# Kernel tuning notes

Measured on AMD Instinct MI355X. Metric: run time of the kernel, lower is better.

Reference implementation:

```python
import jax, jax.numpy as jnp
import numpy as np

QLEN, KLEN, BSZ, NHEAD, DHEAD = 1024, 1024, 2, 16, 64
RLEN = QLEN + KLEN
SCALE = 1.0 / np.sqrt(DHEAD).astype(np.float32)  # 1/sqrt(d_head)


def setup_inputs() -> dict:
    key = jax.random.key(0)
    ks = jax.random.split(key, 10)
    return {
        "q_head": jax.random.normal(ks[0], (QLEN, BSZ, NHEAD, DHEAD), jnp.float32),
        "k_head_h": jax.random.normal(ks[1], (KLEN, BSZ, NHEAD, DHEAD), jnp.float32),
        "v_head_h": jax.random.normal(ks[2], (KLEN, BSZ, NHEAD, DHEAD), jnp.float32),
        "k_head_r": jax.random.normal(ks[3], (RLEN, BSZ, NHEAD, DHEAD), jnp.float32),
        "seg_embed": jax.random.normal(ks[4], (2, NHEAD, DHEAD), jnp.float32),
        "seg_mat": jax.random.uniform(ks[5], (QLEN, KLEN, BSZ, 2), jnp.float32),
        "r_w_bias": jax.random.normal(ks[6], (NHEAD, DHEAD), jnp.float32),
        "r_r_bias": jax.random.normal(ks[7], (NHEAD, DHEAD), jnp.float32),
        "r_s_bias": jax.random.normal(ks[8], (NHEAD, DHEAD), jnp.float32),
        "attn_mask": jnp.zeros((QLEN, KLEN, 1, 1), jnp.float32),
    }


def _rel_shift(x, klen):
    # x: [qlen, rlen, bsz, n_head] -> [qlen, klen, bsz, n_head]
    x = jnp.transpose(x, (1, 0, 2, 3))[1:]          # drop first position row
    x = jnp.transpose(x, (1, 0, 2, 3))[:, :klen]    # keep first klen columns
    return x


def reference(q_head, k_head_h, v_head_h, k_head_r, seg_embed, seg_mat,
              r_w_bias, r_r_bias, r_s_bias, attn_mask):
    # content-based score
    ac = jnp.einsum('ibnd,jbnd->ijbn', q_head + r_w_bias, k_head_h)
    # position-based score with relative shift
    bd = jnp.einsum('ibnd,jbnd->ijbn', q_head + r_r_bias, k_head_r)
    bd = _rel_shift(bd, klen=ac.shape[1])
    # segment-based score
    ef = jnp.einsum('ibnd,snd->ibns', q_head + r_s_bias, seg_embed)
    ef = jnp.einsum('ijbs,ibns->ijbn', seg_mat, ef)
    attn_score = (ac + bd + ef) * SCALE
    attn_score = attn_score - 1e30 * attn_mask
    attn_prob = jax.nn.softmax(attn_score, axis=1)  # over key dim j
    attn_vec = jnp.einsum('ijbn,jbnd->ibnd', attn_prob, v_head_h)
    return attn_vec
```

## Files before the change

kernel.cpp:

```cpp
#include <hip/hip_runtime.h>

#define QLEN 1024
#define KLEN 1024
#define BSZ 2
#define NHEAD 16
#define DHEAD 64
#define RS 2048
#define BLK_I 64
#define BLK_J 32
#define NT32 (KLEN / BLK_J)
#define NBN (BSZ * NHEAD)

#define SC2f  0.18033688011112440f
#define MBIGf 1.4426950408889634e30f
#define THRf  8.0f

#define SEGP_BYTES  16777216u
#define KT_BYTES    ((size_t)NBN * NT32 * 4096)
#define OPART_BYTES 16777216u
#define ML_BYTES    524288u

typedef __attribute__((ext_vector_type(8))) short s16x8;
typedef __attribute__((ext_vector_type(4))) short s16x4;
typedef __attribute__((ext_vector_type(8))) unsigned short u16x8;
typedef __attribute__((ext_vector_type(4))) unsigned short u16x4;
typedef __attribute__((ext_vector_type(4))) float f32x4;
typedef __attribute__((ext_vector_type(2))) float f32x2;

__device__ __forceinline__ unsigned short f2bf(float f) {
    union { float f; unsigned int u; } x; x.f = f;
    unsigned int r = x.u + 0x7fffu + ((x.u >> 16) & 1u);
    return (unsigned short)(r >> 16);
}
__device__ __forceinline__ float bf2f(unsigned short h) {
    union { unsigned int u; float f; } x; x.u = ((unsigned int)h) << 16;
    return x.f;
}

__device__ __forceinline__ f32x4 mfma16x16x16(s16x4 a, s16x4 b, f32x4 c) {
#if __has_builtin(__builtin_amdgcn_mfma_f32_16x16x16bf16_1k)
    return __builtin_amdgcn_mfma_f32_16x16x16bf16_1k(a, b, c, 0, 0, 0);
#else
    f32x4 d;
    asm("v_mfma_f32_16x16x16_bf16 %0, %1, %2, %3"
        : "=v"(d) : "v"(a), "v"(b), "0"(c));
    return d;
#endif
}

typedef const __attribute__((address_space(1))) unsigned int* gas_t;
typedef __attribute__((address_space(3))) unsigned int* las_t;
__device__ __forceinline__ void gl_lds16(const void* g, void* l) {
    __builtin_amdgcn_global_load_lds((gas_t)g, (las_t)l, 16, 0, 0);
}

__global__ __launch_bounds__(256)
void pack_all_kernel(const float* __restrict__ segmat,
                     const float* __restrict__ mask,
                     const float* __restrict__ kh,
                     const float* __restrict__ kr,
                     const float* __restrict__ v,
                     unsigned short* __restrict__ segT,
                     unsigned short* __restrict__ Kp,
                     unsigned short* __restrict__ Krp,
                     unsigned short* __restrict__ Vtp)
{
    __shared__ float smS[16][32][4];
    __shared__ float smM[16][33];
    __shared__ float VT[32][65];
    const int bid = blockIdx.x;
    const int tid = threadIdx.x;

    if (bid < 2048) {
        const int istrip = bid >> 5;
        const int jt     = bid & 31;
        const int ib     = istrip * 16;
        const int jb     = jt * 32;
        {
            const int il = tid >> 4;
            const int j2 = (tid & 15) * 2;
            const float* sp = segmat + ((size_t)(ib + il) * KLEN + jb + j2) * 4;
            *(f32x4*)&smS[il][j2][0]     = *(const f32x4*)sp;
            *(f32x4*)&smS[il][j2 + 1][0] = *(const f32x4*)(sp + 4);
            const float* mp = mask + (size_t)(ib + il) * KLEN + jb + j2;
            smM[il][j2]     = mp[0] * MBIGf;
            smM[il][j2 + 1] = mp[1] * MBIGf;
        }
        __syncthreads();
        const int k  = tid >> 6;
        const int l  = tid & 63;
        const int q4 = l >> 4;
        const int il = l & 15;
        const int jl = (k >> 1) * 16 + q4 * 4 + (k & 1) * 2;
#pragma unroll
        for (int b = 0; b < 2; ++b) {
            u16x8 o;
#pragma unroll
            for (int e = 0; e < 2; ++e) {
                o[e * 4 + 0] = f2bf(smS[il][jl + e][b * 2]);
                o[e * 4 + 1] = f2bf(smS[il][jl + e][b * 2 + 1]);
                o[e * 4 + 2] = f2bf(smM[il][jl + e]);
                o[e * 4 + 3] = 0;
            }
            unsigned short* op = segT + ((size_t)(b * 64 + istrip) << 16)
                                 + (jt << 11) + tid * 8;
            *(u16x8*)op = o;
        }
    } else {
        const int blk = bid - 2048;
        const int bn  = blk >> 5;
        const int jt  = blk & (NT32 - 1);
        const int b   = bn & 1;
        const int n   = bn >> 1;
        const int boff = b * NHEAD * DHEAD + n * DHEAD;
        const int j0  = jt * BLK_J;

        {
            const int j  = tid >> 3;
            const int dq = (tid & 7) * 8;
            const float* vp = v + (size_t)(j0 + j) * RS + boff + dq;
#pragma unroll
            for (int e = 0; e < 8; ++e) VT[j][dq + e] = vp[e];
        }
        __syncthreads();

        const size_t tb = (size_t)blk * 2048;
        {
            const int row = tid >> 3;
            const int ch  = (tid & 7) ^ (row & 7);
            u16x8 ok, orr;
            const float* hp = kh + (size_t)(j0 + row) * RS + boff + ch * 8;
            const float* rp = kr + (size_t)(j0 + row + 1) * RS + boff + ch * 8;
#pragma unroll
            for (int e = 0; e < 8; ++e) { ok[e] = f2bf(hp[e]); orr[e] = f2bf(rp[e]); }
            *(u16x8*)&Kp [tb + (size_t)tid * 8] = ok;
            *(u16x8*)&Krp[tb + (size_t)tid * 8] = orr;
        }
        {
            const int d  = tid >> 2;
            const int g  = tid & 3;
            const int ch = g ^ (d & 3);
            u16x8 ov;
#pragma unroll
            for (int e = 0; e < 8; ++e) ov[e] = f2bf(VT[ch * 8 + e][d]);
            *(u16x8*)&Vtp[tb + (size_t)tid * 8] = ov;
        }
    }
}

__global__ __launch_bounds__(256)
void merge_kernel(const float* __restrict__ opart,
                  const float* __restrict__ ml,
                  float* __restrict__ out)
{
    const int gid = blockIdx.x * 256 + threadIdx.x;
    const int d   = gid & 63;
    const int rr  = gid >> 6;
    const int i   = rr & (QLEN - 1);
    const int n   = (rr >> 10) & (NHEAD - 1);
    const int b   = rr >> 14;
    const int r0  = rr;
    const int r1  = (NBN * QLEN) + rr;
    const float m0 = ml[r0 * 2], l0 = ml[r0 * 2 + 1];
    const float m1 = ml[r1 * 2], l1 = ml[r1 * 2 + 1];
    const float M  = fmaxf(m0, m1);
    const float w0 = __builtin_amdgcn_exp2f(m0 - M);
    const float w1 = __builtin_amdgcn_exp2f(m1 - M);
    const float inv = 1.f / (l0 * w0 + l1 * w1);
    const float o = (opart[(size_t)r0 * 64 + d] * w0 + opart[(size_t)r1 * 64 + d] * w1) * inv;
    out[(size_t)i * RS + b * NHEAD * DHEAD + n * DHEAD + d] = o;
}

__global__ __launch_bounds__(256, 4)
void relattn_kernel(const float* __restrict__ q,
                    const float* __restrict__ segemb,
                    const float* __restrict__ rwb,
                    const float* __restrict__ rrb,
                    const float* __restrict__ rsb,
                    const unsigned short* __restrict__ segT,
                    const unsigned short* __restrict__ Kp,
                    const unsigned short* __restrict__ Krp,
                    const unsigned short* __restrict__ Vtp,
                    float* __restrict__ opart,
                    float* __restrict__ mlpart,
                    float* __restrict__ out,
                    int jsplit, int njt)
{
    __shared__ unsigned short KhL[2][32][64];
    __shared__ unsigned short KrL[2][32][64];
    __shared__ unsigned short VtL[2][64][32];

    const int F = blockIdx.x;
    const int x = F & 7;
    const int k = F >> 3;
    const int g = (k >> 4) * 8 + x;
    const int n = k & 15;
    int i0, b, jsp;
    if (jsplit) { i0 = (g >> 2) * BLK_I; b = (g >> 1) & 1; jsp = g & 1; }
    else        { i0 = (g >> 1) * BLK_I; b = g & 1;        jsp = 0;    }
    const int bn = n * 2 + b;
    const int boff = b * NHEAD * DHEAD + n * DHEAD;

    const int tid  = threadIdx.x;
    const int wave = tid >> 6;
    const int lane = tid & 63;
    const int q4   = lane >> 4;
    const int c    = lane & 15;
    const int iRow = i0 + wave * 16 + c;

    s16x8 qwf[2], qrf[2];
    float e0, e1;
    {
        const float* qp = q + (size_t)iRow * RS + boff;
        float es0 = 0.f, es1 = 0.f;
#pragma unroll
        for (int kk = 0; kk < 2; ++kk) {
            const int off = kk * 32 + q4 * 8;
            const f32x4 q0 = *(const f32x4*)(qp + off);
            const f32x4 q1 = *(const f32x4*)(qp + off + 4);
            const f32x4 w0 = *(const f32x4*)(rwb + n * DHEAD + off);
            const f32x4 w1 = *(const f32x4*)(rwb + n * DHEAD + off + 4);
            const f32x4 r0 = *(const f32x4*)(rrb + n * DHEAD + off);
            const f32x4 r1 = *(const f32x4*)(rrb + n * DHEAD + off + 4);
            const f32x4 sa = *(const f32x4*)(segemb + n * DHEAD + off);
            const f32x4 sb = *(const f32x4*)(segemb + n * DHEAD + off + 4);
            const f32x4 ta = *(const f32x4*)(segemb + (NHEAD + n) * DHEAD + off);
            const f32x4 tb = *(const f32x4*)(segemb + (NHEAD + n) * DHEAD + off + 4);
            const f32x4 ra = *(const f32x4*)(rsb + n * DHEAD + off);
            const f32x4 rb = *(const f32x4*)(rsb + n * DHEAD + off + 4);
            s16x8 tw, tr;
#pragma unroll
            for (int e = 0; e < 4; ++e) {
                tw[e]     = (short)f2bf(q0[e] + w0[e]);
                tw[4 + e] = (short)f2bf(q1[e] + w1[e]);
                tr[e]     = (short)f2bf(q0[e] + r0[e]);
                tr[4 + e] = (short)f2bf(q1[e] + r1[e]);
                es0 += (q0[e] + ra[e]) * sa[e] + (q1[e] + rb[e]) * sb[e];
                es1 += (q0[e] + ra[e]) * ta[e] + (q1[e] + rb[e]) * tb[e];
            }
            qwf[kk] = tw; qrf[kk] = tr;
        }
        es0 += __shfl_xor(es0, 16, 64); es0 += __shfl_xor(es0, 32, 64);
        es1 += __shfl_xor(es1, 16, 64); es1 += __shfl_xor(es1, 32, 64);
        e0 = es0 * SC2f; e1 = es1 * SC2f;
    }

    const int tbase = bn * NT32 + jsp * njt;
    auto stage = [&](int jt, int buf) {
        const size_t toff = ((size_t)(tbase + jt)) << 12;
        const int go = tid * 16;
        const int lo = wave * 1024;
        gl_lds16((const char*)Kp  + toff + go, (char*)&KhL[buf][0][0] + lo);
        gl_lds16((const char*)Krp + toff + go, (char*)&KrL[buf][0][0] + lo);
        gl_lds16((const char*)Vtp + toff + go, (char*)&VtL[buf][0][0] + lo);
    };

    stage(0, 0);
    __syncthreads();

    float m = -INFINITY, lsum = 0.f;
    f32x4 acc[4];
#pragma unroll
    for (int dt = 0; dt < 4; ++dt) acc[dt] = (f32x4)0.f;

    const unsigned short* segW = segT + ((size_t)(b * 64 + (i0 >> 4) + wave) << 16);

    int cur = 0;
    for (int jt = 0; jt < njt; ++jt) {
        if (jt + 1 < njt) stage(jt + 1, cur ^ 1);

        const unsigned short* st = segW + ((jsp * njt + jt) << 11);
        u16x8 pg[2][2];
        pg[0][0] = *(const u16x8*)(st + lane * 8);
        pg[0][1] = *(const u16x8*)(st + 512 + lane * 8);
        pg[1][0] = *(const u16x8*)(st + 1024 + lane * 8);
        pg[1][1] = *(const u16x8*)(st + 1536 + lane * 8);

        f32x4 sjT[2];
        sjT[0] = (f32x4)0.f; sjT[1] = (f32x4)0.f;
        __builtin_amdgcn_s_setprio(1);
#pragma unroll
        for (int kk = 0; kk < 2; ++kk)
#pragma unroll
            for (int js = 0; js < 2; ++js) {
                const int row = js * 16 + c;
                const int pcK = ((kk * 4 + q4) ^ (c & 7)) * 8;
                const s16x8 khf = *(const s16x8*)&KhL[cur][row][pcK];
                const s16x8 krf = *(const s16x8*)&KrL[cur][row][pcK];
                sjT[js] = __builtin_amdgcn_mfma_f32_16x16x32_bf16(khf, qwf[kk], sjT[js], 0, 0, 0);
                sjT[js] = __builtin_amdgcn_mfma_f32_16x16x32_bf16(krf, qrf[kk], sjT[js], 0, 0, 0);
            }
        __builtin_amdgcn_s_setprio(0);

        float sc8[8];
#pragma unroll
        for (int js = 0; js < 2; ++js)
#pragma unroll
            for (int r = 0; r < 4; ++r) {
                const u16x8 g2 = pg[js][r >> 1];
                const int bb = (r & 1) * 4;
                sc8[js * 4 + r] = sjT[js][r] * SC2f
                                  + bf2f(g2[bb]) * e0 + bf2f(g2[bb + 1]) * e1
                                  - bf2f(g2[bb + 2]);
            }
        float pmax = fmaxf(
            fmaxf(fmaxf(sc8[0], sc8[1]), fmaxf(sc8[2], sc8[3])),
            fmaxf(fmaxf(sc8[4], sc8[5]), fmaxf(sc8[6], sc8[7])));

        if (!__all(pmax <= m + THRf)) {
            float mt = pmax;
            mt = fmaxf(mt, __shfl_xor(mt, 16, 64));
            mt = fmaxf(mt, __shfl_xor(mt, 32, 64));
            const float mn  = fmaxf(m, mt);
            const float scl = __builtin_amdgcn_exp2f(m - mn);
            m = mn;
            lsum *= scl;
#pragma unroll
            for (int dt = 0; dt < 4; ++dt) acc[dt] *= scl;
        }

        float p[8], ps = 0.f;
#pragma unroll
        for (int e = 0; e < 8; ++e) {
            p[e] = __builtin_amdgcn_exp2f(sc8[e] - m);
            ps += p[e];
        }
        lsum += ps;

        s16x4 pf4[2];
#pragma unroll
        for (int js = 0; js < 2; ++js) {
            union { unsigned int w[2]; s16x4 v; } pk;
            asm("v_cvt_pk_bf16_f32 %0, %1, %2" : "=v"(pk.w[0]) : "v"(p[js * 4 + 0]), "v"(p[js * 4 + 1]));
            asm("v_cvt_pk_bf16_f32 %0, %1, %2" : "=v"(pk.w[1]) : "v"(p[js * 4 + 2]), "v"(p[js * 4 + 3]));
            pf4[js] = pk.v;
        }
        __builtin_amdgcn_s_setprio(1);
#pragma unroll
        for (int dt = 0; dt < 4; ++dt) {
            const unsigned short* vrow = &VtL[cur][dt * 16 + c][0];
#pragma unroll
            for (int js = 0; js < 2; ++js) {
                const int gg = (js * 2 + (q4 >> 1)) ^ (c & 3);
                const s16x4 vf = *(const s16x4*)(vrow + gg * 8 + (q4 & 1) * 4);
                acc[dt] = mfma16x16x16(vf, pf4[js], acc[dt]);
            }
        }
        __builtin_amdgcn_s_setprio(0);

        __syncthreads();
        cur ^= 1;
    }

    lsum += __shfl_xor(lsum, 16, 64);
    lsum += __shfl_xor(lsum, 32, 64);

    if (jsplit) {
        const int rowG = ((jsp * BSZ + b) * NHEAD + n) * QLEN + iRow;
#pragma unroll
        for (int dt = 0; dt < 4; ++dt)
            *(f32x4*)&opart[(size_t)rowG * 64 + dt * 16 + q4 * 4] = acc[dt];
        if (q4 == 0) {
            mlpart[(size_t)rowG * 2]     = m;
            mlpart[(size_t)rowG * 2 + 1] = lsum;
        }
    } else {
        const float inv = 1.f / lsum;
        float* op = out + (size_t)iRow * RS + boff;
#pragma unroll
        for (int dt = 0; dt < 4; ++dt) {
            const f32x4 o = acc[dt] * inv;
            *(f32x4*)&op[dt * 16 + q4 * 4] = o;
        }
    }
}

extern "C" void kernel_launch(void* const* d_in, const int* in_sizes, int n_in,
                              void* d_out, int out_size, void* d_ws, size_t ws_size,
                              hipStream_t stream) {
    const float* q   = (const float*)d_in[0];
    const float* kh  = (const float*)d_in[1];
    const float* v   = (const float*)d_in[2];
    const float* kr  = (const float*)d_in[3];
    const float* se  = (const float*)d_in[4];
    const float* sm  = (const float*)d_in[5];
    const float* rwb = (const float*)d_in[6];
    const float* rrb = (const float*)d_in[7];
    const float* rsb = (const float*)d_in[8];
    const float* msk = (const float*)d_in[9];
    float* out = (float*)d_out;

    char* wsb = (char*)d_ws;
    unsigned short* segT = (unsigned short*)wsb;
    unsigned short* Kp   = (unsigned short*)(wsb + SEGP_BYTES);
    unsigned short* Krp  = (unsigned short*)(wsb + SEGP_BYTES + KT_BYTES);
    unsigned short* Vtp  = (unsigned short*)(wsb + SEGP_BYTES + 2 * KT_BYTES);
    float* opart  = (float*)(wsb + SEGP_BYTES + 3 * KT_BYTES);
    float* mlpart = (float*)(wsb + SEGP_BYTES + 3 * KT_BYTES + OPART_BYTES);

    const int jsplit = (ws_size >= (size_t)SEGP_BYTES + 3 * KT_BYTES + OPART_BYTES + ML_BYTES) ? 1 : 0;
    const int njt    = jsplit ? NT32 / 2 : NT32;

    pack_all_kernel<<<2048 + NBN * NT32, 256, 0, stream>>>(sm, msk, kh, kr, v,
                                                           segT, Kp, Krp, Vtp);
    relattn_kernel<<<jsplit ? 1024 : 512, 256, 0, stream>>>(q, se, rwb, rrb, rsb,
                                                            segT, Kp, Krp, Vtp,
                                                            opart, mlpart, out,
                                                            jsplit, njt);
    if (jsplit)
        merge_kernel<<<NBN * QLEN * DHEAD / 256, 256, 0, stream>>>(opart, mlpart, out);
}
```

Before: 59.60 us.

## Triple-buffer K/V tiles with prefetched segment data and fine-grained vmcnt waits

Moves the K/Kr/Vt LDS staging from double to triple buffering, issuing loads two tiles ahead. The segment-matrix loads are now prefetched one tile ahead into alternating register sets. The full __syncthreads is replaced by explicit vmcnt waits plus s_barrier, so outstanding global loads can stay in flight across iterations. It also folds the softmax scale into the bf16 Q operands and re-swizzles the Vt layout to 4-element chunks to change LDS bank conflicts. The costs are more LDS and registers per block, which may lower occupancy, and the hand-counted vmcnt values are fragile. The loop now assumes an even tile count.

```diff
diff --git a/kernel.cpp b/kernel.cpp
--- a/kernel.cpp
+++ b/kernel.cpp
@@ -138,12 +138,16 @@
         }
         {
             const int d  = tid >> 2;
-            const int g  = tid & 3;
-            const int ch = g ^ (d & 3);
-            u16x8 ov;
-#pragma unroll
-            for (int e = 0; e < 8; ++e) ov[e] = f2bf(VT[ch * 8 + e][d]);
-            *(u16x8*)&Vtp[tb + (size_t)tid * 8] = ov;
+            const int gl = tid & 3;
+#pragma unroll
+            for (int s = 0; s < 2; ++s) {
+                const int gj8 = gl * 2 + s;
+                const int ph  = gj8 ^ (d & 7);
+                u16x4 ov;
+#pragma unroll
+                for (int e = 0; e < 4; ++e) ov[e] = f2bf(VT[gj8 * 4 + e][d]);
+                *(u16x4*)&Vtp[tb + (size_t)d * 32 + ph * 4] = ov;
+            }
         }
     }
 }
@@ -186,9 +190,9 @@
                     float* __restrict__ out,
                     int jsplit, int njt)
 {
-    __shared__ unsigned short KhL[2][32][64];
-    __shared__ unsigned short KrL[2][32][64];
-    __shared__ unsigned short VtL[2][64][32];
+    __shared__ unsigned short KhL[3][32][64];
+    __shared__ unsigned short KrL[3][32][64];
+    __shared__ unsigned short VtL[3][64][32];
 
     const int F = blockIdx.x;
     const int x = F & 7;
@@ -231,10 +235,10 @@
             s16x8 tw, tr;
 #pragma unroll
             for (int e = 0; e < 4; ++e) {
-                tw[e]     = (short)f2bf(q0[e] + w0[e]);
-                tw[4 + e] = (short)f2bf(q1[e] + w1[e]);
-                tr[e]     = (short)f2bf(q0[e] + r0[e]);
-                tr[4 + e] = (short)f2bf(q1[e] + r1[e]);
+                tw[e]     = (short)f2bf((q0[e] + w0[e]) * SC2f);
+                tw[4 + e] = (short)f2bf((q1[e] + w1[e]) * SC2f);
+                tr[e]     = (short)f2bf((q0[e] + r0[e]) * SC2f);
+                tr[4 + e] = (short)f2bf((q1[e] + r1[e]) * SC2f);
                 es0 += (q0[e] + ra[e]) * sa[e] + (q1[e] + rb[e]) * sb[e];
                 es1 += (q0[e] + ra[e]) * ta[e] + (q1[e] + rb[e]) * tb[e];
             }
@@ -254,27 +258,40 @@
         gl_lds16((const char*)Krp + toff + go, (char*)&KrL[buf][0][0] + lo);
         gl_lds16((const char*)Vtp + toff + go, (char*)&VtL[buf][0][0] + lo);
     };
-
-    stage(0, 0);
-    __syncthreads();
+    const unsigned short* segW = segT + ((size_t)(b * 64 + (i0 >> 4) + wave) << 16);
+    auto segload = [&](int jt, u16x8 (&pg)[4]) {
+        const unsigned short* st = segW + ((jsp * njt + jt) << 11);
+        pg[0] = *(const u16x8*)(st + lane * 8);
+        pg[1] = *(const u16x8*)(st + 512 + lane * 8);
+        pg[2] = *(const u16x8*)(st + 1024 + lane * 8);
+        pg[3] = *(const u16x8*)(st + 1536 + lane * 8);
+    };
 
     float m = -INFINITY, lsum = 0.f;
     f32x4 acc[4];
 #pragma unroll
     for (int dt = 0; dt < 4; ++dt) acc[dt] = (f32x4)0.f;
 
-    const unsigned short* segW = segT + ((size_t)(b * 64 + (i0 >> 4) + wave) << 16);
+    u16x8 pgA[4], pgB[4];
+    stage(0, 0);
+    __builtin_amdgcn_sched_barrier(0);
+    segload(0, pgA);
+    __builtin_amdgcn_sched_barrier(0);
+    stage(1, 1);
+    __builtin_amdgcn_sched_barrier(0);
+    asm volatile("s_waitcnt vmcnt(7)" ::: "memory");
+    __builtin_amdgcn_s_barrier();
+    __builtin_amdgcn_sched_barrier(0);
 
     int cur = 0;
-    for (int jt = 0; jt < njt; ++jt) {
-        if (jt + 1 < njt) stage(jt + 1, cur ^ 1);
-
-        const unsigned short* st = segW + ((jsp * njt + jt) << 11);
-        u16x8 pg[2][2];
-        pg[0][0] = *(const u16x8*)(st + lane * 8);
-        pg[0][1] = *(const u16x8*)(st + 512 + lane * 8);
-        pg[1][0] = *(const u16x8*)(st + 1024 + lane * 8);
-        pg[1][1] = *(const u16x8*)(st + 1536 + lane * 8);
+    auto body = [&](int t, u16x8 (&pgC)[4], u16x8 (&pgN)[4]) {
+        const int tn1 = (t + 1 < njt) ? t + 1 : njt - 1;
+        const int tn2 = (t + 2 < njt) ? t + 2 : njt - 1;
+        int b2 = cur + 2; if (b2 >= 3) b2 -= 3;
+        segload(tn1, pgN);
+        __builtin_amdgcn_sched_barrier(0);
+        stage(tn2, b2);
+        __builtin_amdgcn_sched_barrier(0);
 
         f32x4 sjT[2];
         sjT[0] = (f32x4)0.f; sjT[1] = (f32x4)0.f;
@@ -297,9 +314,9 @@
         for (int js = 0; js < 2; ++js)
 #pragma unroll
             for (int r = 0; r < 4; ++r) {
-                const u16x8 g2 = pg[js][r >> 1];
+                const u16x8 g2 = pgC[js * 2 + (r >> 1)];
                 const int bb = (r & 1) * 4;
-                sc8[js * 4 + r] = sjT[js][r] * SC2f
+                sc8[js * 4 + r] = sjT[js][r]
                                   + bf2f(g2[bb]) * e0 + bf2f(g2[bb + 1]) * e1
                                   - bf2f(g2[bb + 2]);
             }
@@ -330,10 +347,10 @@
         s16x4 pf4[2];
 #pragma unroll
         for (int js = 0; js < 2; ++js) {
-            union { unsigned int w[2]; s16x4 v; } pk;
-            asm("v_cvt_pk_bf16_f32 %0, %1, %2" : "=v"(pk.w[0]) : "v"(p[js * 4 + 0]), "v"(p[js * 4 + 1]));
-            asm("v_cvt_pk_bf16_f32 %0, %1, %2" : "=v"(pk.w[1]) : "v"(p[js * 4 + 2]), "v"(p[js * 4 + 3]));
-            pf4[js] = pk.v;
+            union { unsigned int w[2]; s16x4 v; } pk2;
+            asm("v_cvt_pk_bf16_f32 %0, %1, %2" : "=v"(pk2.w[0]) : "v"(p[js*4+0]), "v"(p[js*4+1]));
+            asm("v_cvt_pk_bf16_f32 %0, %1, %2" : "=v"(pk2.w[1]) : "v"(p[js*4+2]), "v"(p[js*4+3]));
+            pf4[js] = pk2.v;
         }
         __builtin_amdgcn_s_setprio(1);
 #pragma unroll
@@ -341,16 +358,24 @@
             const unsigned short* vrow = &VtL[cur][dt * 16 + c][0];
 #pragma unroll
             for (int js = 0; js < 2; ++js) {
-                const int gg = (js * 2 + (q4 >> 1)) ^ (c & 3);
-                const s16x4 vf = *(const s16x4*)(vrow + gg * 8 + (q4 & 1) * 4);
+                const int ph = (js * 4 + q4) ^ (c & 7);
+                const s16x4 vf = *(const s16x4*)(vrow + ph * 4);
                 acc[dt] = mfma16x16x16(vf, pf4[js], acc[dt]);
             }
         }
         __builtin_amdgcn_s_setprio(0);
 
-        __syncthreads();
-        cur ^= 1;
+        asm volatile("s_waitcnt vmcnt(3)" ::: "memory");
+        __builtin_amdgcn_s_barrier();
+        __builtin_amdgcn_sched_barrier(0);
+        ++cur; if (cur >= 3) cur = 0;
+    };
+
+    for (int o = 0; o < njt / 2; ++o) {
+        body(2 * o + 0, pgA, pgB);
+        body(2 * o + 1, pgB, pgA);
     }
+    asm volatile("s_waitcnt vmcnt(0)" ::: "memory");
 
     lsum += __shfl_xor(lsum, 16, 64);
     lsum += __shfl_xor(lsum, 32, 64);
```

New measurement: 59.50 us. Within noise of the previous version (-0.2%).
